# Kernel optimization log

Measured on AMD Instinct MI355X. Metric: run time of the kernel, lower is better.

## Reference

```python
import math
import jax, jax.numpy as jnp
import numpy as np

B, S, DIM_OBS, DIM_ACT = 4, 512, 64, 8
D, NH, DH, FF, L = 1024, 16, 64, 4096, 6


def _ln(x, g, b, eps=1e-5):
    m = x.mean(-1, keepdims=True)
    v = ((x - m) ** 2).mean(-1, keepdims=True)
    return (x - m) / jnp.sqrt(v + eps) * g + b


def _pe(n, d):
    pos = jnp.arange(n, dtype=jnp.float32)[:, None]
    div = jnp.exp(jnp.arange(0, d, 2, dtype=jnp.float32) * (-math.log(10000.0) / d))
    pe = jnp.zeros((n, d), jnp.float32)
    pe = pe.at[:, 0::2].set(jnp.sin(pos * div))
    pe = pe.at[:, 1::2].set(jnp.cos(pos * div))
    return pe


def setup_inputs() -> dict:
    key = jax.random.key(0)
    ks = iter(jax.random.split(key, 40))
    n = lambda shape: jax.random.normal(next(ks), shape, jnp.float32) * 0.02
    return {
        "observations": jax.random.normal(next(ks), (B, S, DIM_OBS), jnp.float32),
        "actions": jax.random.normal(next(ks), (B, S, DIM_ACT), jnp.float32),
        "attn_mask": jnp.ones((B, S), jnp.bool_),
        "W_obs": n((D, DIM_OBS)), "b_obs": jnp.zeros((D,), jnp.float32),
        "W_act": n((D, DIM_ACT)), "b_act": jnp.zeros((D,), jnp.float32),
        "ln0_g": jnp.ones((D,), jnp.float32), "ln0_b": jnp.zeros((D,), jnp.float32),
        "Wq": n((L, D, D)), "Wk": n((L, D, D)), "Wv": n((L, D, D)),
        "Wo": n((L, D, D)), "bo": jnp.zeros((L, D), jnp.float32),
        "ln1_g": jnp.ones((L, D), jnp.float32), "ln1_b": jnp.zeros((L, D), jnp.float32),
        "Wf1": n((L, FF, D)), "bf1": jnp.zeros((L, FF), jnp.float32),
        "Wf2": n((L, D, FF)), "bf2": jnp.zeros((L, D), jnp.float32),
        "W_pred": n((DIM_ACT, S * D)), "b_pred": jnp.zeros((DIM_ACT,), jnp.float32),
    }


def reference(observations, actions, attn_mask, W_obs, b_obs, W_act, b_act,
              ln0_g, ln0_b, Wq, Wk, Wv, Wo, bo, ln1_g, ln1_b,
              Wf1, bf1, Wf2, bf2, W_pred, b_pred):
    b, s = observations.shape[:2]
    pe = _pe(s, D)
    obs_e = observations @ W_obs.T + b_obs + pe
    act_e = actions @ W_act.T + b_act + pe
    # interleave obs/act tokens -> (B, 2S, D)
    x = jnp.stack([obs_e, act_e], axis=2).reshape(b, 2 * s, D)
    x = _ln(x, ln0_g, ln0_b)
    m = ~attn_mask  # ones in -> all-False mask (no-op fill), matching original
    m2 = jnp.stack([m, m], axis=2).reshape(b, 2 * s)[:, None, None, :]
    scale = 1.0 / jnp.sqrt(jnp.float32(DH))

    def layer(h, p):
        wq, wk, wv, wo, bo_, g1, b1_, wf1, bf1_, wf2, bf2_ = p
        t = h.shape[1]
        q = (h @ wq.T).reshape(b, t, NH, DH)
        k = (h @ wk.T).reshape(b, t, NH, DH)
        v = (h @ wv.T).reshape(b, t, NH, DH)
        a = jnp.einsum('bqhd,bkhd->bhqk', q, k) * scale
        a = jnp.where(m2, -1e9, a)
        # FAITHFUL BUG: original multiplies unnormalized scores by V (softmax unused)
        av = jnp.einsum('bhqk,bkhd->bqhd', a, v).reshape(b, t, D)
        attn_out = av @ wo.T + bo_
        h1 = _ln(h + attn_out, g1, b1_)
        f = jax.nn.gelu(h1 @ wf1.T + bf1_, approximate=False)
        # FAITHFUL BUG: layer returns raw ffn output (no residual / ln2)
        return f @ wf2.T + bf2_, None

    x, _ = jax.lax.scan(layer, x, (Wq, Wk, Wv, Wo, bo, ln1_g, ln1_b, Wf1, bf1, Wf2, bf2))
    dec_act = x.reshape(b, s, 2, D)[:, :, 1, :].reshape(b, s * D)
    return jnp.tanh(dec_act @ W_pred.T + b_pred)
```

## Files before the change

kernel.cpp:

```cpp
#include <hip/hip_runtime.h>

typedef __attribute__((ext_vector_type(8))) _Float16 half8;
typedef __attribute__((ext_vector_type(4))) _Float16 half4v;
typedef __attribute__((ext_vector_type(4))) float f32x4;

__device__ __forceinline__ void gload16(const void* g, void* l) {
  __builtin_amdgcn_global_load_lds((__attribute__((address_space(1))) void*)(g),
                                   (__attribute__((address_space(3))) void*)(l), 16, 0, 0);
}

__global__ __launch_bounds__(256) void embed_kernel(
    const float* __restrict__ obs, const float* __restrict__ act,
    const float* __restrict__ W_obs, const float* __restrict__ b_obs,
    const float* __restrict__ W_act, const float* __restrict__ b_act,
    float* __restrict__ e) {
  const int row = blockIdx.x;
  const int b = row >> 10, t = row & 1023;
  const int pos = t >> 1;
  const bool is_act = t & 1;
  __shared__ float in_row[64];
  const int tid = threadIdx.x;
  if (!is_act) { if (tid < 64) in_row[tid] = obs[(size_t)(b * 512 + pos) * 64 + tid]; }
  else         { if (tid < 8)  in_row[tid] = act[(size_t)(b * 512 + pos) * 8 + tid]; }
  __syncthreads();
  for (int d = tid; d < 1024; d += 256) {
    float acc;
    if (!is_act) {
      acc = b_obs[d];
      const float* w = &W_obs[d * 64];
      #pragma unroll 8
      for (int c = 0; c < 64; ++c) acc += in_row[c] * w[c];
    } else {
      acc = b_act[d];
      const float* w = &W_act[d * 8];
      #pragma unroll
      for (int c = 0; c < 8; ++c) acc += in_row[c] * w[c];
    }
    const int j = d >> 1;
    const float dv = expf((float)(2 * j) * (-9.210340371976184f / 1024.0f));
    const float ang = (float)pos * dv;
    acc += (d & 1) ? cosf(ang) : sinf(ang);
    e[(size_t)row * 1024 + d] = acc;
  }
}

template<bool RES, bool WF32>
__global__ __launch_bounds__(256) void ln_kernel(
    const float* __restrict__ in, const float* __restrict__ res,
    const float* __restrict__ g, const float* __restrict__ bta,
    float* __restrict__ of, _Float16* __restrict__ ohh, _Float16* __restrict__ ohl) {
  const int row = blockIdx.x;
  const size_t base = (size_t)row * 1024;
  const int tid = threadIdx.x;
  float v[4];
  {
    const f32x4 a = *(const f32x4*)&in[base + tid * 4];
    if (RES) {
      const f32x4 r = *(const f32x4*)&res[base + tid * 4];
      v[0] = a[0] + r[0]; v[1] = a[1] + r[1]; v[2] = a[2] + r[2]; v[3] = a[3] + r[3];
    } else {
      v[0] = a[0]; v[1] = a[1]; v[2] = a[2]; v[3] = a[3];
    }
  }
  float s = 0.f, sq = 0.f;
  #pragma unroll
  for (int c = 0; c < 4; ++c) { s += v[c]; sq += v[c] * v[c]; }
  #pragma unroll
  for (int off = 32; off; off >>= 1) { s += __shfl_down(s, off); sq += __shfl_down(sq, off); }
  __shared__ float rs[4], rq[4];
  const int wid = tid >> 6, lane = tid & 63;
  if (!lane) { rs[wid] = s; rq[wid] = sq; }
  __syncthreads();
  s = rs[0] + rs[1] + rs[2] + rs[3];
  sq = rq[0] + rq[1] + rq[2] + rq[3];
  const float mean = s * (1.f / 1024.f);
  const float var = sq * (1.f / 1024.f) - mean * mean;
  const float rstd = rsqrtf(var + 1e-5f);
  #pragma unroll
  for (int c = 0; c < 4; ++c) {
    const int d = tid * 4 + c;
    const float o = (v[c] - mean) * rstd * g[d] + bta[d];
    if (WF32) of[base + d] = o;
    const _Float16 hi = (_Float16)o;
    ohh[base + d] = hi;
    ohl[base + d] = (_Float16)(o - (float)hi);
  }
}

__global__ __launch_bounds__(256) void f2h_split_kernel(const float* __restrict__ s,
                                                        _Float16* __restrict__ hi,
                                                        _Float16* __restrict__ lo, int n) {
  int i = (blockIdx.x * 256 + threadIdx.x) * 4;
  const int stride = gridDim.x * 256 * 4;
  for (; i < n; i += stride) {
    const f32x4 v = *(const f32x4*)&s[i];
    half4v h, l;
    #pragma unroll
    for (int c = 0; c < 4; ++c) {
      h[c] = (_Float16)v[c];
      l[c] = (_Float16)(v[c] - (float)h[c]);
    }
    *(half4v*)&hi[i] = h;
    *(half4v*)&lo[i] = l;
  }
}

template<bool BIAS, bool GELU, bool WF32, bool WF16>
__global__ __launch_bounds__(256, 2) void gemm_bt(
    const _Float16* __restrict__ Ah, const _Float16* __restrict__ Al,
    const _Float16* __restrict__ Bh, const _Float16* __restrict__ Bl,
    const float* __restrict__ bias,
    float* __restrict__ Cf, _Float16* __restrict__ Chh, _Float16* __restrict__ Chl,
    const int M, const int N, const int K) {
  __shared__ _Float16 lds[2][4][4096];
  const int tid = threadIdx.x;
  const int wid = tid >> 6, lane = tid & 63;
  const int wm = wid >> 1, wn = wid & 1;
  const int m0 = blockIdx.y * 128, n0 = blockIdx.x * 128;
  const int KT = K >> 5;

  f32x4 acc[4][4];
  #pragma unroll
  for (int i = 0; i < 4; ++i)
    #pragma unroll
    for (int j = 0; j < 4; ++j) acc[i][j] = f32x4{0.f, 0.f, 0.f, 0.f};

  const int ho0 = wid * 512 + lane * 8;
  const int r0s = ho0 >> 5, kk0 = ho0 & 31;
  const int ho1 = (wid + 4) * 512 + lane * 8;
  const int r1s = ho1 >> 5, kk1 = ho1 & 31;

  auto stage = [&](int buf, int kt) {
    const int k0 = kt << 5;
    const size_t a0 = (size_t)(m0 + r0s) * K + k0 + kk0;
    const size_t a1 = (size_t)(m0 + r1s) * K + k0 + kk1;
    const size_t b0 = (size_t)(n0 + r0s) * K + k0 + kk0;
    const size_t b1 = (size_t)(n0 + r1s) * K + k0 + kk1;
    gload16(Ah + a0, &lds[buf][0][ho0]); gload16(Ah + a1, &lds[buf][0][ho1]);
    gload16(Al + a0, &lds[buf][1][ho0]); gload16(Al + a1, &lds[buf][1][ho1]);
    gload16(Bh + b0, &lds[buf][2][ho0]); gload16(Bh + b1, &lds[buf][2][ho1]);
    gload16(Bl + b0, &lds[buf][3][ho0]); gload16(Bl + b1, &lds[buf][3][ho1]);
  };

  stage(0, 0);
  int cur = 0;
  const int lr = lane & 15, lk = (lane >> 4) * 8;
  for (int kt = 0; kt < KT; ++kt) {
    __syncthreads();
    if (kt + 1 < KT) stage(cur ^ 1, kt + 1);
    const _Float16* lAh = &lds[cur][0][0];
    const _Float16* lAl = &lds[cur][1][0];
    const _Float16* lBh = &lds[cur][2][0];
    const _Float16* lBl = &lds[cur][3][0];
    half8 afh[4], afl[4], bfh[4], bfl[4];
    #pragma unroll
    for (int mi = 0; mi < 4; ++mi) {
      const int o = (wm * 64 + mi * 16 + lr) * 32 + lk;
      afh[mi] = *(const half8*)&lAh[o];
      afl[mi] = *(const half8*)&lAl[o];
    }
    #pragma unroll
    for (int ni = 0; ni < 4; ++ni) {
      const int o = (wn * 64 + ni * 16 + lr) * 32 + lk;
      bfh[ni] = *(const half8*)&lBh[o];
      bfl[ni] = *(const half8*)&lBl[o];
    }
    #pragma unroll
    for (int mi = 0; mi < 4; ++mi)
      #pragma unroll
      for (int ni = 0; ni < 4; ++ni) {
        acc[mi][ni] = __builtin_amdgcn_mfma_f32_16x16x32_f16(afh[mi], bfh[ni], acc[mi][ni], 0, 0, 0);
        acc[mi][ni] = __builtin_amdgcn_mfma_f32_16x16x32_f16(afl[mi], bfh[ni], acc[mi][ni], 0, 0, 0);
        acc[mi][ni] = __builtin_amdgcn_mfma_f32_16x16x32_f16(afh[mi], bfl[ni], acc[mi][ni], 0, 0, 0);
      }
    cur ^= 1;
  }

  const int lq = lane >> 4;
  #pragma unroll
  for (int mi = 0; mi < 4; ++mi) {
    const int gr = m0 + wm * 64 + mi * 16 + lq * 4;
    #pragma unroll
    for (int ni = 0; ni < 4; ++ni) {
      const int gc = n0 + wn * 64 + ni * 16 + lr;
      float bv = 0.f;
      if (BIAS) bv = bias[gc];
      #pragma unroll
      for (int j = 0; j < 4; ++j) {
        float v = acc[mi][ni][j] + bv;
        if (GELU) v = 0.5f * v * (1.f + erff(v * 0.70710678118654752f));
        const size_t o = (size_t)(gr + j) * N + gc;
        if (WF32) Cf[o] = v;
        if (WF16) {
          const _Float16 hi = (_Float16)v;
          Chh[o] = hi;
          Chl[o] = (_Float16)(v - (float)hi);
        }
      }
    }
  }
}

__global__ __launch_bounds__(256) void ktv_kernel(const _Float16* __restrict__ qh,
                                                  const _Float16* __restrict__ ql,
                                                  float* __restrict__ Mp) {
  const int bid = blockIdx.x;
  const int q = bid & 3, bh = bid >> 2;
  const int b = bh >> 4, h = bh & 15;
  __shared__ float Ks[8192], Vs[8192];
  const int tid = threadIdx.x;
  const int tq = tid >> 6;
  const int tile = tid & 63;
  const int i0 = (tile >> 3) * 8, j0 = (tile & 7) * 8;
  float acc[8][8];
  #pragma unroll
  for (int ii = 0; ii < 8; ++ii)
    #pragma unroll
    for (int jj = 0; jj < 8; ++jj) acc[ii][jj] = 0.f;

  for (int cc = 0; cc < 2; ++cc) {
    const int c = q * 2 + cc;
    for (int idx = tid * 8; idx < 8192; idx += 2048) {
      const int r = idx >> 6, kk = idx & 63;
      const size_t g = (size_t)(b * 1024 + c * 128 + r) * 3072 + h * 64 + kk;
      const half8 k_h = *(const half8*)&qh[g + 1024];
      const half8 k_l = *(const half8*)&ql[g + 1024];
      const half8 v_h = *(const half8*)&qh[g + 2048];
      const half8 v_l = *(const half8*)&ql[g + 2048];
      #pragma unroll
      for (int xx = 0; xx < 8; ++xx) {
        Ks[idx + xx] = (float)k_h[xx] + (float)k_l[xx];
        Vs[idx + xx] = (float)v_h[xx] + (float)v_l[xx];
      }
    }
    __syncthreads();
    for (int r = tq * 32; r < tq * 32 + 32; ++r) {
      float kv[8], vv[8];
      #pragma unroll
      for (int xx = 0; xx < 8; ++xx) { kv[xx] = Ks[r * 64 + i0 + xx]; vv[xx] = Vs[r * 64 + j0 + xx]; }
      #pragma unroll
      for (int ii = 0; ii < 8; ++ii)
        #pragma unroll
        for (int jj = 0; jj < 8; ++jj) acc[ii][jj] += kv[ii] * vv[jj];
    }
    __syncthreads();
  }
  __shared__ float red[64][64];
  for (int pp = 0; pp < 4; ++pp) {
    if (tq == pp) {
      #pragma unroll
      for (int ii = 0; ii < 8; ++ii)
        #pragma unroll
        for (int jj = 0; jj < 8; ++jj) {
          if (pp == 0) red[tile][ii * 8 + jj] = acc[ii][jj];
          else         red[tile][ii * 8 + jj] += acc[ii][jj];
        }
    }
    __syncthreads();
  }
  for (int o = tid; o < 4096; o += 256) {
    const int i = o >> 6, j = o & 63;
    Mp[((size_t)(q * 64 + bh) << 12) + o] = red[(i >> 3) * 8 + (j >> 3)][(i & 7) * 8 + (j & 7)];
  }
}

__global__ __launch_bounds__(256) void av_kernel(const _Float16* __restrict__ qh,
                                                 const _Float16* __restrict__ ql,
                                                 const float* __restrict__ Mp,
                                                 _Float16* __restrict__ avh,
                                                 _Float16* __restrict__ avl) {
  const int id = blockIdx.x;
  const int tc = id & 7, bh = id >> 3;
  const int b = bh >> 4, h = bh & 15;
  __shared__ float Ms[4096];
  __shared__ float Qs[8192];
  const int tid = threadIdx.x;
  for (int o = tid * 4; o < 4096; o += 1024) {
    const f32x4 p0 = *(const f32x4*)&Mp[((size_t)(bh) << 12) + o];
    const f32x4 p1 = *(const f32x4*)&Mp[((size_t)(64 + bh) << 12) + o];
    const f32x4 p2 = *(const f32x4*)&Mp[((size_t)(128 + bh) << 12) + o];
    const f32x4 p3 = *(const f32x4*)&Mp[((size_t)(192 + bh) << 12) + o];
    f32x4 m;
    #pragma unroll
    for (int c = 0; c < 4; ++c) m[c] = 0.125f * (p0[c] + p1[c] + p2[c] + p3[c]);
    *(f32x4*)&Ms[o] = m;
  }
  for (int idx = tid * 8; idx < 8192; idx += 2048) {
    const int r = idx >> 6, kk = idx & 63;
    const size_t g = (size_t)(b * 1024 + tc * 128 + r) * 3072 + h * 64 + kk;
    const half8 q_h = *(const half8*)&qh[g];
    const half8 q_l = *(const half8*)&ql[g];
    #pragma unroll
    for (int xx = 0; xx < 8; ++xx) Qs[idx + xx] = (float)q_h[xx] + (float)q_l[xx];
  }
  __syncthreads();
  const int r0 = (tid >> 3) * 4, j0 = (tid & 7) * 8;
  float acc[4][8];
  #pragma unroll
  for (int rr = 0; rr < 4; ++rr)
    #pragma unroll
    for (int jj = 0; jj < 8; ++jj) acc[rr][jj] = 0.f;
  for (int i = 0; i < 64; ++i) {
    float m8[8];
    #pragma unroll
    for (int jj = 0; jj < 8; ++jj) m8[jj] = Ms[i * 64 + j0 + jj];
    #pragma unroll
    for (int rr = 0; rr < 4; ++rr) {
      const float qv = Qs[(r0 + rr) * 64 + i];
      #pragma unroll
      for (int jj = 0; jj < 8; ++jj) acc[rr][jj] += qv * m8[jj];
    }
  }
  #pragma unroll
  for (int rr = 0; rr < 4; ++rr)
    #pragma unroll
    for (int jj = 0; jj < 8; ++jj) {
      const size_t o = (size_t)(b * 1024 + tc * 128 + r0 + rr) * 1024 + h * 64 + j0 + jj;
      const float v = acc[rr][jj];
      const _Float16 hi = (_Float16)v;
      avh[o] = hi;
      avl[o] = (_Float16)(v - (float)hi);
    }
}

__global__ __launch_bounds__(256) void pred_kernel(const float* __restrict__ x,
                                                   const float* __restrict__ Wp,
                                                   const float* __restrict__ bp,
                                                   float* __restrict__ out) {
  const int b = blockIdx.x >> 3, a = blockIdx.x & 7;
  const int tid = threadIdx.x;
  float acc = 0.f;
  for (int i4 = tid * 4; i4 < 524288; i4 += 1024) {
    const int s = i4 >> 10, d = i4 & 1023;
    const f32x4 xv = *(const f32x4*)&x[(size_t)(b * 1024 + 2 * s + 1) * 1024 + d];
    const f32x4 wv = *(const f32x4*)&Wp[(size_t)a * 524288 + i4];
    acc += xv[0] * wv[0] + xv[1] * wv[1] + xv[2] * wv[2] + xv[3] * wv[3];
  }
  #pragma unroll
  for (int off = 32; off; off >>= 1) acc += __shfl_down(acc, off);
  __shared__ float red[4];
  const int wid = tid >> 6, lane = tid & 63;
  if (!lane) red[wid] = acc;
  __syncthreads();
  if (tid == 0) out[b * 8 + a] = tanhf(red[0] + red[1] + red[2] + red[3] + bp[a]);
}

extern "C" void kernel_launch(void* const* d_in, const int* in_sizes, int n_in,
                              void* d_out, int out_size, void* d_ws, size_t ws_size,
                              hipStream_t stream) {
  (void)in_sizes; (void)n_in; (void)out_size; (void)ws_size;
  const float* obs    = (const float*)d_in[0];
  const float* act    = (const float*)d_in[1];
  const float* W_obs  = (const float*)d_in[3];
  const float* b_obs  = (const float*)d_in[4];
  const float* W_act  = (const float*)d_in[5];
  const float* b_act  = (const float*)d_in[6];
  const float* ln0_g  = (const float*)d_in[7];
  const float* ln0_b  = (const float*)d_in[8];
  const float* Wq     = (const float*)d_in[9];
  const float* Wk     = (const float*)d_in[10];
  const float* Wv     = (const float*)d_in[11];
  const float* Wo     = (const float*)d_in[12];
  const float* bo     = (const float*)d_in[13];
  const float* ln1_g  = (const float*)d_in[14];
  const float* ln1_b  = (const float*)d_in[15];
  const float* Wf1    = (const float*)d_in[16];
  const float* bf1    = (const float*)d_in[17];
  const float* Wf2    = (const float*)d_in[18];
  const float* bf2    = (const float*)d_in[19];
  const float* W_pred = (const float*)d_in[20];
  const float* b_pred = (const float*)d_in[21];
  float* out = (float*)d_out;

  char* p = (char*)d_ws;
  auto alloc = [&](size_t bytes) { char* r = p; p += (bytes + 255) & ~(size_t)255; return r; };
  const size_t MB = 1024 * 1024;
  _Float16* whqkv_h = (_Float16*)alloc(6 * MB);
  _Float16* whqkv_l = (_Float16*)alloc(6 * MB);
  _Float16* who_h   = (_Float16*)alloc(2 * MB);
  _Float16* who_l   = (_Float16*)alloc(2 * MB);
  _Float16* whf1_h  = (_Float16*)alloc(8 * MB);
  _Float16* whf1_l  = (_Float16*)alloc(8 * MB);
  _Float16* whf2_h  = (_Float16*)alloc(8 * MB);
  _Float16* whf2_l  = (_Float16*)alloc(8 * MB);
  float*    e       = (float*)alloc(16 * MB);
  float*    x       = (float*)alloc(16 * MB);
  _Float16* xh_h    = (_Float16*)alloc(8 * MB);
  _Float16* xh_l    = (_Float16*)alloc(8 * MB);
  _Float16* av_h    = (_Float16*)alloc(8 * MB);
  _Float16* av_l    = (_Float16*)alloc(8 * MB);
  _Float16* h1_h    = (_Float16*)alloc(8 * MB);
  _Float16* h1_l    = (_Float16*)alloc(8 * MB);
  float*    Mp      = (float*)alloc(4 * MB);
  char*     U       = alloc(64 * MB);
  _Float16* qkv_h = (_Float16*)U;
  _Float16* qkv_l = (_Float16*)(U + 24 * MB);
  _Float16* fh_h  = (_Float16*)U;
  _Float16* fh_l  = (_Float16*)(U + 32 * MB);
  float* ao = e;

  auto f2h = [&](const float* s, _Float16* hh, _Float16* ll, int n) {
    int blocks = (n / 4 + 255) / 256; if (blocks > 2048) blocks = 2048;
    f2h_split_kernel<<<blocks, 256, 0, stream>>>(s, hh, ll, n);
  };

  embed_kernel<<<4096, 256, 0, stream>>>(obs, act, W_obs, b_obs, W_act, b_act, e);
  ln_kernel<false, true><<<4096, 256, 0, stream>>>(e, nullptr, ln0_g, ln0_b, x, xh_h, xh_l);

  for (int l = 0; l < 6; ++l) {
    const size_t dd = (size_t)l * 1024 * 1024, df = (size_t)l * 4096 * 1024;
    f2h(Wq + dd, whqkv_h,           whqkv_l,           1048576);
    f2h(Wk + dd, whqkv_h + 1048576, whqkv_l + 1048576, 1048576);
    f2h(Wv + dd, whqkv_h + 2097152, whqkv_l + 2097152, 1048576);
    f2h(Wo + dd, who_h,  who_l,  1048576);
    f2h(Wf1 + df, whf1_h, whf1_l, 4194304);
    f2h(Wf2 + df, whf2_h, whf2_l, 4194304);

    gemm_bt<false, false, false, true><<<dim3(24, 32), 256, 0, stream>>>(
        xh_h, xh_l, whqkv_h, whqkv_l, nullptr, nullptr, qkv_h, qkv_l, 4096, 3072, 1024);
    ktv_kernel<<<256, 256, 0, stream>>>(qkv_h, qkv_l, Mp);
    av_kernel<<<512, 256, 0, stream>>>(qkv_h, qkv_l, Mp, av_h, av_l);
    gemm_bt<true, false, true, false><<<dim3(8, 32), 256, 0, stream>>>(
        av_h, av_l, who_h, who_l, bo + (size_t)l * 1024, ao, nullptr, nullptr, 4096, 1024, 1024);
    ln_kernel<true, false><<<4096, 256, 0, stream>>>(
        x, ao, ln1_g + (size_t)l * 1024, ln1_b + (size_t)l * 1024, nullptr, h1_h, h1_l);
    gemm_bt<true, true, false, true><<<dim3(32, 32), 256, 0, stream>>>(
        h1_h, h1_l, whf1_h, whf1_l, bf1 + (size_t)l * 4096, nullptr, fh_h, fh_l, 4096, 4096, 1024);
    gemm_bt<true, false, true, true><<<dim3(8, 32), 256, 0, stream>>>(
        fh_h, fh_l, whf2_h, whf2_l, bf2 + (size_t)l * 1024, x, xh_h, xh_l, 4096, 1024, 4096);
  }

  pred_kernel<<<32, 256, 0, stream>>>(x, W_pred, b_pred, out);
}
```

Measured before the change: 3.252 ms.

## Remap GEMM workgroups across XCDs and split prediction reduction over many blocks

The GEMM kernel now remaps its flat workgroup index so consecutive tiles are grouped per XCD (stride of nwg/8). The aim is better L2 reuse of A/B tiles on the multi-die GPU. Separately, the final prediction GEMV goes from 32 blocks to a two-stage reduction: 2048 blocks write partial sums, then a small kernel reduces them and applies tanh. This raises parallelism for a memory-bound reduction at the cost of one extra launch.

```diff
diff --git a/kernel.cpp b/kernel.cpp
--- a/kernel.cpp
+++ b/kernel.cpp
@@ -116,7 +116,11 @@
   const int tid = threadIdx.x;
   const int wid = tid >> 6, lane = tid & 63;
   const int wm = wid >> 1, wn = wid & 1;
-  const int m0 = blockIdx.y * 128, n0 = blockIdx.x * 128;
+
+  const int nwg = gridDim.x * gridDim.y;
+  int flat = blockIdx.y * gridDim.x + blockIdx.x;
+  flat = (flat & 7) * (nwg >> 3) + (flat >> 3);
+  const int m0 = (flat / gridDim.x) * 128, n0 = (flat % gridDim.x) * 128;
   const int KT = K >> 5;
 
   f32x4 acc[4][4];
@@ -323,14 +327,17 @@
     }
 }
 
-__global__ __launch_bounds__(256) void pred_kernel(const float* __restrict__ x,
+__global__ __launch_bounds__(256) void pred_split1(const float* __restrict__ x,
                                                    const float* __restrict__ Wp,
-                                                   const float* __restrict__ bp,
-                                                   float* __restrict__ out) {
-  const int b = blockIdx.x >> 3, a = blockIdx.x & 7;
-  const int tid = threadIdx.x;
+                                                   float* __restrict__ partial) {
+  const int bid = blockIdx.x;
+  const int b = bid >> 9, a = (bid >> 6) & 7, sp = bid & 63;
+  const int tid = threadIdx.x;
+  const int base = sp * 8192;
   float acc = 0.f;
-  for (int i4 = tid * 4; i4 < 524288; i4 += 1024) {
+  #pragma unroll
+  for (int it = 0; it < 8; ++it) {
+    const int i4 = base + it * 1024 + tid * 4;
     const int s = i4 >> 10, d = i4 & 1023;
     const f32x4 xv = *(const f32x4*)&x[(size_t)(b * 1024 + 2 * s + 1) * 1024 + d];
     const f32x4 wv = *(const f32x4*)&Wp[(size_t)a * 524288 + i4];
@@ -342,7 +349,18 @@
   const int wid = tid >> 6, lane = tid & 63;
   if (!lane) red[wid] = acc;
   __syncthreads();
-  if (tid == 0) out[b * 8 + a] = tanhf(red[0] + red[1] + red[2] + red[3] + bp[a]);
+  if (tid == 0) partial[bid] = red[0] + red[1] + red[2] + red[3];
+}
+
+__global__ __launch_bounds__(64) void pred_split2(const float* __restrict__ partial,
+                                                  const float* __restrict__ bp,
+                                                  float* __restrict__ out) {
+  const int pair = blockIdx.x;
+  const int lane = threadIdx.x;
+  float v = partial[pair * 64 + lane];
+  #pragma unroll
+  for (int off = 32; off; off >>= 1) v += __shfl_down(v, off);
+  if (lane == 0) out[pair] = tanhf(v + bp[pair & 7]);
 }
 
 extern "C" void kernel_launch(void* const* d_in, const int* in_sizes, int n_in,
@@ -392,6 +410,7 @@
   _Float16* h1_h    = (_Float16*)alloc(8 * MB);
   _Float16* h1_l    = (_Float16*)alloc(8 * MB);
   float*    Mp      = (float*)alloc(4 * MB);
+  float*    pred_p  = (float*)alloc(2048 * 4);
   char*     U       = alloc(64 * MB);
   _Float16* qkv_h = (_Float16*)U;
   _Float16* qkv_l = (_Float16*)(U + 24 * MB);
@@ -430,5 +449,6 @@
         fh_h, fh_l, whf2_h, whf2_l, bf2 + (size_t)l * 1024, x, xh_h, xh_l, 4096, 1024, 4096);
   }
 
-  pred_kernel<<<32, 256, 0, stream>>>(x, W_pred, b_pred, out);
-}
+  pred_split1<<<2048, 256, 0, stream>>>(x, W_pred, pred_p);
+  pred_split2<<<32, 64, 0, stream>>>(pred_p, b_pred, out);
+}
```

After: 2.731 ms. 1.19x faster.
